# Optimization experiments

Measured on AMD Instinct MI355X. Metric: run time of the kernel, lower is better.

## Reference

```python
import jax, jax.numpy as jnp
import numpy as np

N, FEATS, HIDDEN, CLASSES, E, DEPTH = 100000, 512, 64, 64, 3200000, 10


def setup_inputs() -> dict:
    key = jax.random.key(0)
    ks = jax.random.split(key, 8)
    x = jax.random.normal(ks[0], (N, FEATS), jnp.float32)
    edges = jax.random.randint(ks[1], (2, E), 0, N, jnp.int32)
    mask = jax.random.randint(ks[2], (N,), 0, 2, jnp.int32)
    labels = jax.random.randint(ks[3], (N,), 0, CLASSES, jnp.int32)
    s1 = 1.0 / np.sqrt(FEATS)
    s2 = 1.0 / np.sqrt(HIDDEN)
    w1 = jax.random.uniform(ks[4], (FEATS, HIDDEN), jnp.float32, -s1, s1)
    b1 = jax.random.uniform(ks[5], (HIDDEN,), jnp.float32, -s1, s1)
    w2 = jax.random.uniform(ks[6], (HIDDEN, CLASSES), jnp.float32, -s2, s2)
    b2 = jax.random.uniform(ks[7], (CLASSES,), jnp.float32, -s2, s2)
    return {"x": x, "w1": w1, "b1": b1, "w2": w2, "b2": b2,
            "edges": edges, "mask": mask, "labels": labels}


def _graph_conv(h, src, dst, norm):
    # out[v] = sum over edges (u -> v) of h[u] / sqrt(deg_out(u) * deg_in(v))
    return jax.ops.segment_sum(h[src] * norm[:, None], dst, num_segments=N)


def reference(x, w1, b1, w2, b2, edges, mask, labels):
    src, dst = edges[0], edges[1]
    ones = jnp.ones((E,), jnp.float32)
    deg_out = jnp.maximum(jax.ops.segment_sum(ones, src, num_segments=N), 1.0)
    deg_in = jnp.maximum(jax.ops.segment_sum(ones, dst, num_segments=N), 1.0)
    norm = jax.lax.rsqrt(deg_out[src] * deg_in[dst])  # [E]

    # eval path: dropout is identity
    h = jax.nn.relu(x @ w1 + b1)
    p = jax.nn.softmax(h @ w2 + b2, axis=1)  # [N, C]

    train = mask != 0  # [N] bool
    onehot = jax.nn.one_hot(labels, CLASSES, dtype=p.dtype) * train[:, None]
    err = onehot - p
    h0 = err
    tm = train[:, None]
    for _ in range(DEPTH):
        err = _graph_conv(err, src, dst, norm)
        err = jnp.where(tm, h0, err)  # err[nz,:] = h0[nz,:]

    out = p + err
    h0 = out
    for _ in range(DEPTH):
        out = _graph_conv(out, src, dst, norm) * 0.9 + h0 * 0.1
    return jnp.log(out + 1.0)
```

## Files before the change

kernel.cpp:

```cpp
#include <hip/hip_runtime.h>
#include <hip/hip_fp16.h>
#include <math.h>

#define NN    100000
#define FEATS 512
#define HID   64
#define EE    3200000
#define WIDTH 96

__global__ void ell_build(const int* __restrict__ src, const int* __restrict__ dst,
                          int* __restrict__ deg_out, int* __restrict__ fill,
                          int* __restrict__ col) {
  int stride = gridDim.x * blockDim.x;
  int tid = blockIdx.x * blockDim.x + threadIdx.x;
  const int4* s4 = reinterpret_cast<const int4*>(src);
  const int4* d4 = reinterpret_cast<const int4*>(dst);
  for (int q = tid; q < EE / 4; q += stride) {
    int4 s = s4[q];
    int4 d = d4[q];
    atomicAdd(&deg_out[s.x], 1);
    atomicAdd(&deg_out[s.y], 1);
    atomicAdd(&deg_out[s.z], 1);
    atomicAdd(&deg_out[s.w], 1);
    int p0 = atomicAdd(&fill[d.x], 1);
    if (p0 < WIDTH) col[(size_t)d.x * WIDTH + p0] = s.x;
    int p1 = atomicAdd(&fill[d.y], 1);
    if (p1 < WIDTH) col[(size_t)d.y * WIDTH + p1] = s.y;
    int p2 = atomicAdd(&fill[d.z], 1);
    if (p2 < WIDTH) col[(size_t)d.z * WIDTH + p2] = s.z;
    int p3 = atomicAdd(&fill[d.w], 1);
    if (p3 < WIDTH) col[(size_t)d.w * WIDTH + p3] = s.w;
  }
}

__global__ void node_prep(const int* __restrict__ dout, const int* __restrict__ din,
                          float* __restrict__ r_out, float* __restrict__ rr,
                          float* __restrict__ inv_r_out) {
  int i = blockIdx.x * 256 + threadIdx.x;
  if (i >= NN) return;
  int a = dout[i]; if (a < 1) a = 1;
  int b = din[i];  if (b < 1) b = 1;
  float ro = rsqrtf((float)a);
  r_out[i] = ro;
  rr[i] = ro * rsqrtf((float)b);
  inv_r_out[i] = sqrtf((float)a);
}

__global__ __launch_bounds__(256) void fused_mlp(const float* __restrict__ x,
                                                 const float* __restrict__ w1,
                                                 const float* __restrict__ b1,
                                                 const float* __restrict__ w2,
                                                 const float* __restrict__ b2,
                                                 const int* __restrict__ mask,
                                                 const int* __restrict__ labels,
                                                 float* __restrict__ p,
                                                 __half* __restrict__ err0) {
  __shared__ float hs[64 * 65];
  __shared__ float w2s[64 * 64];
  float* xs = w2s;
  float* ws = w2s + 64 * 17;
  int t = threadIdx.x;
  int row0 = blockIdx.x * 64;
  int tx = t & 15, ty = t >> 4;
  int lr = t >> 2, lq = t & 3;
  int wk = t >> 4, wc = (t & 15) * 4;
  float acc[4][4] = {};
  for (int k0 = 0; k0 < FEATS; k0 += 16) {
    float4 xv = make_float4(0.f, 0.f, 0.f, 0.f);
    int gr = row0 + lr;
    if (gr < NN) xv = *reinterpret_cast<const float4*>(x + (size_t)gr * FEATS + k0 + lq * 4);
    float4 wv = *reinterpret_cast<const float4*>(w1 + (size_t)(k0 + wk) * HID + wc);
    xs[lr * 17 + lq * 4 + 0] = xv.x; xs[lr * 17 + lq * 4 + 1] = xv.y;
    xs[lr * 17 + lq * 4 + 2] = xv.z; xs[lr * 17 + lq * 4 + 3] = xv.w;
    ws[wk * 64 + wc + 0] = wv.x; ws[wk * 64 + wc + 1] = wv.y;
    ws[wk * 64 + wc + 2] = wv.z; ws[wk * 64 + wc + 3] = wv.w;
    __syncthreads();
#pragma unroll
    for (int kk = 0; kk < 16; ++kk) {
      float a[4], b[4];
#pragma unroll
      for (int ii = 0; ii < 4; ++ii) a[ii] = xs[(ty * 4 + ii) * 17 + kk];
#pragma unroll
      for (int jj = 0; jj < 4; ++jj) b[jj] = ws[kk * 64 + tx * 4 + jj];
#pragma unroll
      for (int ii = 0; ii < 4; ++ii)
#pragma unroll
        for (int jj = 0; jj < 4; ++jj) acc[ii][jj] = fmaf(a[ii], b[jj], acc[ii][jj]);
    }
    __syncthreads();
  }
  float bb[4];
#pragma unroll
  for (int jj = 0; jj < 4; ++jj) bb[jj] = b1[tx * 4 + jj];
#pragma unroll
  for (int ii = 0; ii < 4; ++ii)
#pragma unroll
    for (int jj = 0; jj < 4; ++jj)
      hs[(ty * 4 + ii) * 65 + tx * 4 + jj] = fmaxf(acc[ii][jj] + bb[jj], 0.f);
#pragma unroll
  for (int q = 0; q < 16; ++q) w2s[t + q * 256] = w2[t + q * 256];
  __syncthreads();
  float lg[4][4];
#pragma unroll
  for (int jj = 0; jj < 4; ++jj) {
    float b2v = b2[tx * 4 + jj];
#pragma unroll
    for (int ii = 0; ii < 4; ++ii) lg[ii][jj] = b2v;
  }
#pragma unroll 4
  for (int k = 0; k < 64; ++k) {
    float hk[4];
#pragma unroll
    for (int ii = 0; ii < 4; ++ii) hk[ii] = hs[(ty * 4 + ii) * 65 + k];
#pragma unroll
    for (int jj = 0; jj < 4; ++jj) {
      float wv2 = w2s[k * 64 + tx * 4 + jj];
#pragma unroll
      for (int ii = 0; ii < 4; ++ii) lg[ii][jj] = fmaf(hk[ii], wv2, lg[ii][jj]);
    }
  }
  __syncthreads();
#pragma unroll
  for (int ii = 0; ii < 4; ++ii)
#pragma unroll
    for (int jj = 0; jj < 4; ++jj)
      hs[(ty * 4 + ii) * 65 + tx * 4 + jj] = lg[ii][jj];
  __syncthreads();
  int wv_ = t >> 6, lane = t & 63;
  for (int q = 0; q < 16; ++q) {
    int r = wv_ * 16 + q;
    int i = row0 + r;
    if (i >= NN) break;
    float v = hs[r * 65 + lane];
    float m = v;
#pragma unroll
    for (int off = 32; off >= 1; off >>= 1) m = fmaxf(m, __shfl_xor(m, off));
    float e = expf(v - m);
    float s = e;
#pragma unroll
    for (int off = 32; off >= 1; off >>= 1) s += __shfl_xor(s, off);
    float pv = e / s;
    size_t off64 = (size_t)i * 64 + lane;
    p[off64] = pv;
    float oh = (mask[i] != 0 && labels[i] == lane) ? 1.f : 0.f;
    err0[off64] = __float2half(oh - pv);
  }
}

template <int MODE>
__global__ __launch_bounds__(256) void conv_h(const int* __restrict__ fill,
                                              const int* __restrict__ col,
                                              const float* __restrict__ r_out,
                                              const float* __restrict__ rr,
                                              const float* __restrict__ inv_r_out,
                                              const int* __restrict__ mask,
                                              const __half* __restrict__ in,
                                              const __half* __restrict__ uinit,
                                              __half* __restrict__ out,
                                              float* __restrict__ fout) {
  int wid = (blockIdx.x * 256 + threadIdx.x) >> 6;
  int lane = threadIdx.x & 63;
  if (wid >= NN) return;
  size_t off = (size_t)wid * 64 + lane;
  if (MODE <= 1) {
    if (mask[wid] != 0) {
      if (MODE == 0) out[off] = __float2half(r_out[wid] * __half2float(in[off]));
      else           out[off] = in[off];
      return;
    }
  }
  int cnt = fill[wid];
  if (cnt > WIDTH) cnt = WIDTH;
  const int* cp = col + (size_t)wid * WIDTH;
  float sum = 0.f;
  int e = 0;
  for (; e + 16 <= cnt; e += 16) {
    int cc[16];
#pragma unroll
    for (int j = 0; j < 16; ++j) cc[j] = cp[e + j];
    float vv[16];
#pragma unroll
    for (int j = 0; j < 16; ++j) vv[j] = __half2float(in[(size_t)cc[j] * 64 + lane]);
    if (MODE == 0) {
      float wv[16];
#pragma unroll
      for (int j = 0; j < 16; ++j) wv[j] = r_out[cc[j]];
#pragma unroll
      for (int j = 0; j < 16; ++j) sum = fmaf(wv[j], vv[j], sum);
    } else {
#pragma unroll
      for (int j = 0; j < 16; ++j) sum += vv[j];
    }
  }
  if (e + 8 <= cnt) {
    int cc[8];
#pragma unroll
    for (int j = 0; j < 8; ++j) cc[j] = cp[e + j];
    float vv[8];
#pragma unroll
    for (int j = 0; j < 8; ++j) vv[j] = __half2float(in[(size_t)cc[j] * 64 + lane]);
    if (MODE == 0) {
      float wv[8];
#pragma unroll
      for (int j = 0; j < 8; ++j) wv[j] = r_out[cc[j]];
#pragma unroll
      for (int j = 0; j < 8; ++j) sum = fmaf(wv[j], vv[j], sum);
    } else {
#pragma unroll
      for (int j = 0; j < 8; ++j) sum += vv[j];
    }
    e += 8;
  }
  for (; e < cnt; ++e) {
    int c = cp[e];
    float v = __half2float(in[(size_t)c * 64 + lane]);
    if (MODE == 0) sum = fmaf(r_out[c], v, sum);
    else sum += v;
  }
  if (MODE == 0 || MODE == 1) {
    out[off] = __float2half(rr[wid] * sum);
  } else {
    float f = fmaf(0.9f * rr[wid], sum, 0.1f * __half2float(uinit[off]));
    if (MODE == 2) out[off] = __float2half(f);
    else           fout[off] = logf(f * inv_r_out[wid] + 1.f);
  }
}

__global__ void combine_kernel(const float* __restrict__ p, const __half* __restrict__ t10,
                               const float* __restrict__ r_out, __half* __restrict__ u) {
  int idx = blockIdx.x * 256 + threadIdx.x;
  if (idx >= NN * 32) return;
  int i = idx >> 5;
  float ro = r_out[i];
  float2 pv = reinterpret_cast<const float2*>(p)[idx];
  __half2 tv = reinterpret_cast<const __half2*>(t10)[idx];
  float2 tf = __half22float2(tv);
  reinterpret_cast<__half2*>(u)[idx] =
      __floats2half2_rn(fmaf(ro, pv.x, tf.x), fmaf(ro, pv.y, tf.y));
}

extern "C" void kernel_launch(void* const* d_in, const int* in_sizes, int n_in,
                              void* d_out, int out_size, void* d_ws, size_t ws_size,
                              hipStream_t stream) {
  const float* x      = (const float*)d_in[0];
  const float* w1     = (const float*)d_in[1];
  const float* b1     = (const float*)d_in[2];
  const float* w2     = (const float*)d_in[3];
  const float* b2     = (const float*)d_in[4];
  const int*   edges  = (const int*)d_in[5];
  const int*   mask   = (const int*)d_in[6];
  const int*   labels = (const int*)d_in[7];
  const int*   src = edges;
  const int*   dst = edges + EE;

  char* w = (char*)d_ws;
  auto alloc = [&](size_t bytes) -> char* {
    char* pp = w;
    w += (bytes + 255) & ~(size_t)255;
    return pp;
  };
  int*    deg_out = (int*)alloc((size_t)NN * 4);
  int*    fillc   = (int*)alloc((size_t)NN * 4);
  float*  r_out   = (float*)alloc((size_t)NN * 4);
  float*  rr      = (float*)alloc((size_t)NN * 4);
  float*  inv_ro  = (float*)alloc((size_t)NN * 4);
  float*  P       = (float*)alloc((size_t)NN * HID * 4);
  __half* E       = (__half*)alloc((size_t)NN * HID * 2);
  __half* F       = (__half*)alloc((size_t)NN * HID * 2);
  __half* U       = (__half*)alloc((size_t)NN * HID * 2);
  int*    col     = (int*)alloc((size_t)NN * WIDTH * 4);

  hipMemsetAsync(deg_out, 0, (size_t)((char*)r_out - (char*)deg_out), stream);

  const int SCAN_NB = (NN + 255) / 256;
  const int CONV_GRID = (NN + 3) / 4;

  ell_build<<<2048, 256, 0, stream>>>(src, dst, deg_out, fillc, col);
  fused_mlp<<<(NN + 63) / 64, 256, 0, stream>>>(x, w1, b1, w2, b2, mask, labels, P, E);
  node_prep<<<SCAN_NB, 256, 0, stream>>>(deg_out, fillc, r_out, rr, inv_ro);

#define CONV(MODE, IN, UI, OUT, FOUT)                                              \
  conv_h<MODE><<<CONV_GRID, 256, 0, stream>>>(fillc, col, r_out, rr, inv_ro, mask, \
                                              IN, UI, OUT, FOUT)

  CONV(0, E, (__half*)nullptr, F, (float*)nullptr);
  {
    __half* in = F; __half* out = E;
    for (int it = 0; it < 9; ++it) {
      CONV(1, in, (__half*)nullptr, out, (float*)nullptr);
      __half* tmp = in; in = out; out = tmp;
    }
  }

  combine_kernel<<<(NN * 32 + 255) / 256, 256, 0, stream>>>(P, E, r_out, U);

  CONV(2, U, U, F, (float*)nullptr);
  {
    __half* in = F; __half* out = E;
    for (int it = 1; it < 9; ++it) {
      CONV(2, in, U, out, (float*)nullptr);
      __half* tmp = in; in = out; out = tmp;
    }
  }
  CONV(3, F, U, (__half*)nullptr, (float*)d_out);
#undef CONV
}
```

Before: 2.109 ms.

## Fold source normalization into MLP output and widen conv gather batches

The out-degree rsqrt scaling is applied to the initial error inside the fused MLP kernel. This removes the special first convolution mode, so all ten error-propagation steps use the plain-sum kernel. The conv gather loop is also rewritten to load column indices with int4 vectors and issue 32 neighbor gathers per batch, padding the tail with a duplicate index. The padding adds redundant loads for low-degree nodes in exchange for more memory-level parallelism and fewer loop branches.

New measurement: 2.014 ms. 1.05x faster.

```diff
diff --git a/kernel.cpp b/kernel.cpp
--- a/kernel.cpp
+++ b/kernel.cpp
@@ -53,6 +53,7 @@
                                                  const float* __restrict__ b2,
                                                  const int* __restrict__ mask,
                                                  const int* __restrict__ labels,
+                                                 const float* __restrict__ r_out,
                                                  float* __restrict__ p,
                                                  __half* __restrict__ err0) {
   __shared__ float hs[64 * 65];
@@ -143,14 +144,13 @@
     size_t off64 = (size_t)i * 64 + lane;
     p[off64] = pv;
     float oh = (mask[i] != 0 && labels[i] == lane) ? 1.f : 0.f;
-    err0[off64] = __float2half(oh - pv);
+    err0[off64] = __float2half(r_out[i] * (oh - pv));
   }
 }
 
 template <int MODE>
 __global__ __launch_bounds__(256) void conv_h(const int* __restrict__ fill,
                                               const int* __restrict__ col,
-                                              const float* __restrict__ r_out,
                                               const float* __restrict__ rr,
                                               const float* __restrict__ inv_r_out,
                                               const int* __restrict__ mask,
@@ -162,62 +162,33 @@
   int lane = threadIdx.x & 63;
   if (wid >= NN) return;
   size_t off = (size_t)wid * 64 + lane;
-  if (MODE <= 1) {
-    if (mask[wid] != 0) {
-      if (MODE == 0) out[off] = __float2half(r_out[wid] * __half2float(in[off]));
-      else           out[off] = in[off];
-      return;
-    }
+  if (MODE == 1) {
+    if (mask[wid] != 0) { out[off] = in[off]; return; }
   }
   int cnt = fill[wid];
   if (cnt > WIDTH) cnt = WIDTH;
   const int* cp = col + (size_t)wid * WIDTH;
   float sum = 0.f;
-  int e = 0;
-  for (; e + 16 <= cnt; e += 16) {
-    int cc[16];
-#pragma unroll
-    for (int j = 0; j < 16; ++j) cc[j] = cp[e + j];
-    float vv[16];
-#pragma unroll
-    for (int j = 0; j < 16; ++j) vv[j] = __half2float(in[(size_t)cc[j] * 64 + lane]);
-    if (MODE == 0) {
-      float wv[16];
-#pragma unroll
-      for (int j = 0; j < 16; ++j) wv[j] = r_out[cc[j]];
-#pragma unroll
-      for (int j = 0; j < 16; ++j) sum = fmaf(wv[j], vv[j], sum);
-    } else {
-#pragma unroll
-      for (int j = 0; j < 16; ++j) sum += vv[j];
-    }
-  }
-  if (e + 8 <= cnt) {
-    int cc[8];
-#pragma unroll
-    for (int j = 0; j < 8; ++j) cc[j] = cp[e + j];
-    float vv[8];
-#pragma unroll
-    for (int j = 0; j < 8; ++j) vv[j] = __half2float(in[(size_t)cc[j] * 64 + lane]);
-    if (MODE == 0) {
-      float wv[8];
-#pragma unroll
-      for (int j = 0; j < 8; ++j) wv[j] = r_out[cc[j]];
-#pragma unroll
-      for (int j = 0; j < 8; ++j) sum = fmaf(wv[j], vv[j], sum);
-    } else {
-#pragma unroll
-      for (int j = 0; j < 8; ++j) sum += vv[j];
-    }
-    e += 8;
-  }
-  for (; e < cnt; ++e) {
-    int c = cp[e];
-    float v = __half2float(in[(size_t)c * 64 + lane]);
-    if (MODE == 0) sum = fmaf(r_out[c], v, sum);
-    else sum += v;
-  }
-  if (MODE == 0 || MODE == 1) {
+  for (int e = 0; e < cnt; e += 32) {
+    int cc[32];
+#pragma unroll
+    for (int q = 0; q < 8; ++q) {
+      int4 c4 = *reinterpret_cast<const int4*>(cp + e + q * 4);
+      cc[q * 4 + 0] = c4.x; cc[q * 4 + 1] = c4.y;
+      cc[q * 4 + 2] = c4.z; cc[q * 4 + 3] = c4.w;
+    }
+    int rem = cnt - e;
+    int c0 = cc[0];
+#pragma unroll
+    for (int j = 0; j < 32; ++j)
+      if (j >= rem) cc[j] = c0;
+    float vv[32];
+#pragma unroll
+    for (int j = 0; j < 32; ++j) vv[j] = __half2float(in[(size_t)cc[j] * 64 + lane]);
+#pragma unroll
+    for (int j = 0; j < 32; ++j) sum += (j < rem) ? vv[j] : 0.f;
+  }
+  if (MODE == 1) {
     out[off] = __float2half(rr[wid] * sum);
   } else {
     float f = fmaf(0.9f * rr[wid], sum, 0.1f * __half2float(uinit[off]));
@@ -276,17 +247,17 @@
   const int CONV_GRID = (NN + 3) / 4;
 
   ell_build<<<2048, 256, 0, stream>>>(src, dst, deg_out, fillc, col);
-  fused_mlp<<<(NN + 63) / 64, 256, 0, stream>>>(x, w1, b1, w2, b2, mask, labels, P, E);
   node_prep<<<SCAN_NB, 256, 0, stream>>>(deg_out, fillc, r_out, rr, inv_ro);
-
-#define CONV(MODE, IN, UI, OUT, FOUT)                                              \
-  conv_h<MODE><<<CONV_GRID, 256, 0, stream>>>(fillc, col, r_out, rr, inv_ro, mask, \
+  fused_mlp<<<(NN + 63) / 64, 256, 0, stream>>>(x, w1, b1, w2, b2, mask, labels,
+                                                r_out, P, E);
+
+#define CONV(MODE, IN, UI, OUT, FOUT)                                           \
+  conv_h<MODE><<<CONV_GRID, 256, 0, stream>>>(fillc, col, rr, inv_ro, mask,     \
                                               IN, UI, OUT, FOUT)
 
-  CONV(0, E, (__half*)nullptr, F, (float*)nullptr);
   {
-    __half* in = F; __half* out = E;
-    for (int it = 0; it < 9; ++it) {
+    __half* in = E; __half* out = F;
+    for (int it = 0; it < 10; ++it) {
       CONV(1, in, (__half*)nullptr, out, (float*)nullptr);
       __half* tmp = in; in = out; out = tmp;
     }
```
